# Kernel optimization log

Hardware: AMD Instinct MI355X
Metric: run time of the kernel (lower is better)

The kernel has to match this reference:

```python
import jax, jax.numpy as jnp
import numpy as np

B, N, D = 4096, 64, 12
SS = 5            # self_state_dim
I = D - SS        # lstm input dim = 7
H = 256           # hn_state_dim
M1, M2 = 512, 512 # mlp_dims
A = 81            # n_actions


def setup_inputs() -> dict:
    key = jax.random.key(0)
    ks = jax.random.split(key, 12)
    w = lambda k, shape: (jax.random.normal(k, shape, jnp.float32) * 0.05)
    return {
        "state": jax.random.normal(ks[0], (B, N, D), jnp.float32),
        "W_ih": w(ks[1], (4 * H, I)),
        "W_hh": w(ks[2], (4 * H, H)),
        "b_ih": w(ks[3], (4 * H,)),
        "b_hh": w(ks[4], (4 * H,)),
        "W1": w(ks[5], (SS + H, M1)),
        "b1": w(ks[6], (M1,)),
        "W2": w(ks[7], (M1, M2)),
        "b2": w(ks[8], (M2,)),
        "Wv": w(ks[9], (M2, A)),
        "bv": w(ks[10], (A,)),
    }


def reference(state, W_ih, W_hh, b_ih, b_hh, W1, b1, W2, b2, Wv, bv):
    self_state = state[:, 0, :SS]                      # [B, SS]
    # dist: inf when either of coords 5,6 is zero (faithful to np.all(..)==0 quirk)
    s5, s6 = state[..., 5], state[..., 6]
    d = jnp.where((s5 != 0) & (s6 != 0),
                  jnp.sqrt(s5 * s5 + s6 * s6), jnp.inf)  # [B, N]
    order = jnp.argsort(-d, axis=1)                    # stable desc sort by dist
    sorted_state = jnp.take_along_axis(state, order[..., None], axis=1)
    x = sorted_state[:, :, SS:]                        # [B, N, I]

    def step(carry, xt):
        h, c = carry
        g = xt @ W_ih.T + b_ih + h @ W_hh.T + b_hh     # [B, 4H]
        i, f, gg, o = jnp.split(g, 4, axis=-1)
        c = jax.nn.sigmoid(f) * c + jax.nn.sigmoid(i) * jnp.tanh(gg)
        h = jax.nn.sigmoid(o) * jnp.tanh(c)
        return (h, c), None

    h0 = jnp.zeros((state.shape[0], H), state.dtype)
    (hn, _), _ = jax.lax.scan(step, (h0, h0), jnp.swapaxes(x, 0, 1))

    joint = jnp.concatenate([self_state, hn], axis=1)  # [B, SS+H]
    out = jax.nn.relu(joint @ W1 + b1)
    out = jax.nn.relu(out @ W2 + b2)                   # last_relu=True
    values = out @ Wv + bv                             # [B, A]
    return values
```

## Files before the change

kernel.cpp:

```cpp
#include <hip/hip_runtime.h>
#include <math.h>

#define B_   4096
#define N_   64
#define SS_  5
#define I_   7
#define H_   256
#define M1_  512
#define M2_  512
#define A_   81

typedef _Float16 f16;
typedef f16   f16x8 __attribute__((ext_vector_type(8)));
typedef float f32x4 __attribute__((ext_vector_type(4)));
typedef int   i32x4 __attribute__((ext_vector_type(4)));

__device__ __forceinline__ float sigm_(float x) {
  return __builtin_amdgcn_rcpf(1.f + __expf(-x));
}
__device__ __forceinline__ float tanh_(float x) {
  return 1.f - 2.f * __builtin_amdgcn_rcpf(__expf(2.f * x) + 1.f);
}

__global__ __launch_bounds__(1024) void pack_weights(
    const float* __restrict__ W_ih,
    const float* __restrict__ W_hh,
    const float* __restrict__ b_ih,
    const float* __restrict__ b_hh,
    const float* __restrict__ W1,
    const float* __restrict__ W2,
    const float* __restrict__ Wv,
    signed char* __restrict__ Wq2,
    signed char* __restrict__ Wql2,
    f16* __restrict__ Wxk,
    float* __restrict__ scd,
    f16* __restrict__ Wp1,
    f16* __restrict__ Wp2,
    f16* __restrict__ Wpv) {
  const int gtid = blockIdx.x * 1024 + threadIdx.x;

  if (gtid < 65536) {
    const int p    = gtid >> 6;
    const int lane = gtid & 63;
    const int w16 = p >> 6, r = p & 63, g = r >> 4, uu = r & 15;
    const int row = g * H_ + w16 * 16 + uu;

    const float4 v4 = *(const float4*)(W_hh + row * H_ + lane * 4);
    float mx = fmaxf(fmaxf(fabsf(v4.x), fabsf(v4.y)),
                     fmaxf(fabsf(v4.z), fabsf(v4.w)));
    #pragma unroll
    for (int off = 32; off; off >>= 1)
      mx = fmaxf(mx, __shfl_xor(mx, off));
    mx = fmaxf(mx, 1e-12f);
    const float is = 127.f / mx;

    int b0i = (int)rintf(v4.x * is), b1i = (int)rintf(v4.y * is);
    int b2i = (int)rintf(v4.z * is), b3i = (int)rintf(v4.w * is);
    b0i = max(-127, min(127, b0i)); b1i = max(-127, min(127, b1i));
    b2i = max(-127, min(127, b2i)); b3i = max(-127, min(127, b3i));
    const unsigned int packed = (b0i & 0xff) | ((b1i & 0xff) << 8) |
                                ((b2i & 0xff) << 16) | ((b3i & 0xff) << 24);
    const int k    = lane * 4;
    const int kt2  = k >> 6;
    const int kk   = k & 63;
    *(unsigned int*)(Wq2 + kt2 * 65536 + p * 64 + kk) = packed;

    if (kt2 < 2) {
      const int lgk = kk >> 4;
      const int jq  = kk & 15;
      *(unsigned int*)(Wql2 + ((kt2 * 16 + w16) * 4 + g) * 1024 +
                       lgk * 256 + uu * 16 + jq) = packed;
    }

    if (lane < 8) {
      f16 v;
      if (lane < I_)      v = (f16)W_ih[row * I_ + lane];
      else                v = (f16)(b_ih[row] + b_hh[row]);
      Wxk[p * 8 + lane] = v;
    }
    if (lane == 9)  scd[p] = mx * (1.f / 16129.f);
  }

  if (gtid < 288 * 512) {
    const int k = gtid >> 9, n = gtid & 511;
    const int kt = k >> 5, lg = (k >> 3) & 3, j = k & 7;
    const int nt = n >> 4, l15 = n & 15;
    const float v = (k < 261) ? W1[k * 512 + n] : 0.f;
    Wp1[(((kt * 32 + nt) * 16 + l15) * 4 + lg) * 8 + j] = (f16)v;
  }
  if (gtid < 512 * 512) {
    const int k = gtid >> 9, n = gtid & 511;
    const int kt = k >> 5, lg = (k >> 3) & 3, j = k & 7;
    const int nt = n >> 4, l15 = n & 15;
    Wp2[(((kt * 32 + nt) * 16 + l15) * 4 + lg) * 8 + j] = (f16)W2[k * 512 + n];
  }
  if (gtid < 512 * 96) {
    const int k = gtid / 96, n = gtid - k * 96;
    const int kt = k >> 5, lg = (k >> 3) & 3, j = k & 7;
    const int nt = n >> 4, l15 = n & 15;
    const float v = (n < A_) ? Wv[k * A_ + n] : 0.f;
    Wpv[(((kt * 6 + nt) * 16 + l15) * 4 + lg) * 8 + j] = (f16)v;
  }
}

__global__ void sort_gather(const float* __restrict__ state,
                            f16* __restrict__ xbuf,
                            float* __restrict__ selfbuf) {
  const int b = blockIdx.x;
  const int e = threadIdx.x;
  const float* row = state + ((size_t)b * N_ + e) * 12;
  const float4* r4 = (const float4*)row;
  const float4 v0 = r4[0], v1 = r4[1], v2 = r4[2];
  float s[12];
  s[0]=v0.x; s[1]=v0.y; s[2]=v0.z;  s[3]=v0.w;
  s[4]=v1.x; s[5]=v1.y; s[6]=v1.z;  s[7]=v1.w;
  s[8]=v2.x; s[9]=v2.y; s[10]=v2.z; s[11]=v2.w;

  const float s5 = s[5], s6 = s[6];
  const float d = (s5 != 0.f && s6 != 0.f) ? sqrtf(s5 * s5 + s6 * s6) : INFINITY;

  __shared__ float dd[64];
  dd[e] = d;
  __syncthreads();

  int rank = 0;
  #pragma unroll
  for (int j = 0; j < 64; ++j) {
    const float dj = dd[j];
    rank += (dj > d || (dj == d && j < e)) ? 1 : 0;
  }

  f16* xo = xbuf + (((size_t)(b >> 4) * 64 + rank) * 16 + (b & 15)) * 8;
  #pragma unroll
  for (int f = 0; f < I_; ++f) xo[f] = (f16)s[SS_ + f];
  xo[7] = (f16)1.f;

  if (e == 0) {
    #pragma unroll
    for (int i = 0; i < SS_; ++i) selfbuf[b * SS_ + i] = s[i];
  }
}

__global__ __attribute__((amdgpu_flat_work_group_size(1024, 1024)))
void lstm_kernel(
    const f16* __restrict__ xbuf,
    const signed char* __restrict__ Wq2,
    const signed char* __restrict__ Wql2,
    const f16* __restrict__ Wxk,
    const float* __restrict__ scd,
    float* __restrict__ hnbuf) {
  const int tid = threadIdx.x;
  const int l   = tid & 63;
  const int w   = tid >> 6;
  const int l15 = l & 15;
  const int lg  = l >> 4;
  const int b0  = blockIdx.x << 4;

  extern __shared__ char smem[];
  signed char* Wl_s = (signed char*)smem;
  f16*   Bx_s  = (f16*)(smem + 131072);
  signed char* hq_s = (signed char*)(smem + 147456);
  f16*   x_s   = (f16*)(smem + 155648);

  {
    const f16x8* sw = (const f16x8*)Wql2;
    f16x8* dw = (f16x8*)Wl_s;
    for (int i = tid; i < 8192; i += 1024) dw[i] = sw[i];
    const f16x8* sx = (const f16x8*)Wxk;
    f16x8* dx = (f16x8*)Bx_s;
    for (int i = tid; i < 1024; i += 1024) dx[i] = sx[i];
    for (int i = tid; i < 2048; i += 1024) ((int*)hq_s)[i] = 0;
    if (tid < 128) x_s[tid] = xbuf[(size_t)blockIdx.x * 8192 + tid];
  }

  float scv[4][4];
  #pragma unroll
  for (int g = 0; g < 4; ++g)
    #pragma unroll
    for (int e = 0; e < 4; ++e)
      scv[g][e] = scd[w * 64 + g * 16 + lg * 4 + e];

  const int WLB = w * 4096 + l * 16;
  const int SB  = w * 4096 + l15 * 64 + lg * 16;
  const int BXB = w * 1024 + l15 * 16;
  const int u0  = w * 16 + lg * 4;
  const int HW  = w * 256 + l15 * 16 + lg * 4;
  const int HR  = l * 16;

  i32x4 Bs[2][4];
  #pragma unroll
  for (int m = 0; m < 2; ++m)
    #pragma unroll
    for (int g = 0; g < 4; ++g)
      Bs[m][g] = *(const i32x4*)(Wq2 + (2 + m) * 65536 + g * 1024 + SB);

  float c_[4] = {0.f, 0.f, 0.f, 0.f};

  __syncthreads();

  #pragma unroll 1
  for (int t = 0; t < 64; ++t) {
    int z = 0;
    asm volatile("" : "+v"(z));
    const int wlb = WLB + z;
    const int hrb = HR + ((t & 1) * 4096) + z;
    const int bxb = BXB + z;

    f16 xn = (f16)0.f;
    if (tid < 128) {
      const int tn = (t < 63) ? t + 1 : 63;
      xn = xbuf[(size_t)blockIdx.x * 8192 + tn * 128 + tid];
    }

    f16x8 bx = {(f16)0.f,(f16)0.f,(f16)0.f,(f16)0.f,
                (f16)0.f,(f16)0.f,(f16)0.f,(f16)0.f};
    if (lg == 0) bx = *(const f16x8*)&x_s[(t & 1) * 128 + l15 * 8];

    i32x4 acc[4];
    #pragma unroll
    for (int g = 0; g < 4; ++g) acc[g] = (i32x4){0, 0, 0, 0};

    #pragma unroll
    for (int kt2 = 0; kt2 < 2; ++kt2) {
      const i32x4 Hf = *(const i32x4*)&hq_s[hrb + kt2 * 1024];
      #pragma unroll
      for (int g = 0; g < 4; ++g) {
        const i32x4 Wv = *(const i32x4*)(Wl_s + kt2 * 65536 + g * 1024 + wlb);
        acc[g] = __builtin_amdgcn_mfma_i32_16x16x64_i8(Wv, Hf, acc[g], 0, 0, 0);
      }
    }
    #pragma unroll
    for (int m = 0; m < 2; ++m) {
      const i32x4 Hf = *(const i32x4*)&hq_s[hrb + (2 + m) * 1024];
      #pragma unroll
      for (int g = 0; g < 4; ++g)
        acc[g] = __builtin_amdgcn_mfma_i32_16x16x64_i8(Bs[m][g], Hf, acc[g], 0, 0, 0);
    }

    f32x4 facc[4];
    #pragma unroll
    for (int g = 0; g < 4; ++g) {
      f32x4 accF = (f32x4){0.f, 0.f, 0.f, 0.f};
      const f16x8 Wxv = *(const f16x8*)((const char*)Bx_s + bxb + g * 256);
      accF = __builtin_amdgcn_mfma_f32_16x16x32_f16(Wxv, bx, accF, 0, 0, 0);
      #pragma unroll
      for (int e = 0; e < 4; ++e)
        facc[g][e] = (float)acc[g][e] * scv[g][e] + accF[e];
    }

    float hv[4];
    #pragma unroll
    for (int e = 0; e < 4; ++e) {
      const float gi = facc[0][e];
      const float gf = facc[1][e];
      const float gg = facc[2][e];
      const float go = facc[3][e];
      const float cn = sigm_(gf) * c_[e] + sigm_(gi) * tanh_(gg);
      c_[e] = cn;
      hv[e] = sigm_(go) * tanh_(cn);
    }
    const int q0 = (int)rintf(hv[0] * 127.f) & 255;
    const int q1 = (int)rintf(hv[1] * 127.f) & 255;
    const int q2 = (int)rintf(hv[2] * 127.f) & 255;
    const int q3 = (int)rintf(hv[3] * 127.f) & 255;
    *(unsigned int*)(hq_s + ((t + 1) & 1) * 4096 + HW) =
        (unsigned int)(q0 | (q1 << 8) | (q2 << 16) | (q3 << 24));
    if (t == 63) {
      float4 hx = {hv[0], hv[1], hv[2], hv[3]};
      *(float4*)&hnbuf[(size_t)(b0 + l15) * H_ + u0] = hx;
    }
    if (tid < 128) x_s[((t + 1) & 1) * 128 + tid] = xn;
    __syncthreads();
  }
}

__global__ __launch_bounds__(512) void mlp_kernel(
    const float* __restrict__ selfb, const float* __restrict__ hnbuf,
    const f16* __restrict__ Wp1, const float* __restrict__ b1,
    const f16* __restrict__ Wp2, const float* __restrict__ b2,
    const f16* __restrict__ Wpv, const float* __restrict__ bv,
    float* __restrict__ out) {
  const int tid = threadIdx.x;
  const int l   = tid & 63;
  const int w   = tid >> 6;
  const int l15 = l & 15;
  const int lg  = l >> 4;
  const int b0  = blockIdx.x << 5;

  extern __shared__ char smem[];
  f16* aA = (f16*)smem;
  f16* aB = (f16*)(smem + 18944);
  f16* aC = (f16*)(smem + 18944 + 33280);

  for (int i = tid; i < 32 * 296; i += 512) {
    const int r = i / 296, cc = i - r * 296;
    float v = 0.f;
    if (cc < SS_)        v = selfb[(b0 + r) * SS_ + cc];
    else if (cc < 261)   v = hnbuf[((size_t)(b0 + r)) * H_ + cc - SS_];
    aA[i] = (f16)v;
  }
  __syncthreads();

  f32x4 acc[2][4];

  {
    #pragma unroll
    for (int mt = 0; mt < 2; ++mt)
      #pragma unroll
      for (int nt4 = 0; nt4 < 4; ++nt4) acc[mt][nt4] = (f32x4){0.f,0.f,0.f,0.f};
    for (int kt = 0; kt < 9; ++kt) {
      const f16x8 A0 = *(const f16x8*)&aA[(l15) * 296 + kt * 32 + lg * 8];
      const f16x8 A1 = *(const f16x8*)&aA[(16 + l15) * 296 + kt * 32 + lg * 8];
      #pragma unroll
      for (int nt4 = 0; nt4 < 4; ++nt4) {
        const int nt = w * 4 + nt4;
        const f16x8 Bv = *(const f16x8*)(Wp1 + (((kt * 32 + nt) * 16 + l15) * 4 + lg) * 8);
        acc[0][nt4] = __builtin_amdgcn_mfma_f32_16x16x32_f16(A0, Bv, acc[0][nt4], 0, 0, 0);
        acc[1][nt4] = __builtin_amdgcn_mfma_f32_16x16x32_f16(A1, Bv, acc[1][nt4], 0, 0, 0);
      }
    }
    #pragma unroll
    for (int nt4 = 0; nt4 < 4; ++nt4) {
      const int n = (w * 4 + nt4) * 16 + l15;
      const float bb = b1[n];
      #pragma unroll
      for (int mt = 0; mt < 2; ++mt)
        #pragma unroll
        for (int e = 0; e < 4; ++e) {
          const float v = fmaxf(acc[mt][nt4][e] + bb, 0.f);
          aB[(mt * 16 + lg * 4 + e) * 520 + n] = (f16)v;
        }
    }
  }
  __syncthreads();

  {
    #pragma unroll
    for (int mt = 0; mt < 2; ++mt)
      #pragma unroll
      for (int nt4 = 0; nt4 < 4; ++nt4) acc[mt][nt4] = (f32x4){0.f,0.f,0.f,0.f};
    for (int kt = 0; kt < 16; ++kt) {
      const f16x8 A0 = *(const f16x8*)&aB[(l15) * 520 + kt * 32 + lg * 8];
      const f16x8 A1 = *(const f16x8*)&aB[(16 + l15) * 520 + kt * 32 + lg * 8];
      #pragma unroll
      for (int nt4 = 0; nt4 < 4; ++nt4) {
        const int nt = w * 4 + nt4;
        const f16x8 Bv = *(const f16x8*)(Wp2 + (((kt * 32 + nt) * 16 + l15) * 4 + lg) * 8);
        acc[0][nt4] = __builtin_amdgcn_mfma_f32_16x16x32_f16(A0, Bv, acc[0][nt4], 0, 0, 0);
        acc[1][nt4] = __builtin_amdgcn_mfma_f32_16x16x32_f16(A1, Bv, acc[1][nt4], 0, 0, 0);
      }
    }
    #pragma unroll
    for (int nt4 = 0; nt4 < 4; ++nt4) {
      const int n = (w * 4 + nt4) * 16 + l15;
      const float bb = b2[n];
      #pragma unroll
      for (int mt = 0; mt < 2; ++mt)
        #pragma unroll
        for (int e = 0; e < 4; ++e) {
          const float v = fmaxf(acc[mt][nt4][e] + bb, 0.f);
          aC[(mt * 16 + lg * 4 + e) * 520 + n] = (f16)v;
        }
    }
  }
  __syncthreads();

  if (w < 6) {
    const int n = w * 16 + l15;
    f32x4 acc3[2];
    acc3[0] = (f32x4){0.f,0.f,0.f,0.f};
    acc3[1] = (f32x4){0.f,0.f,0.f,0.f};
    for (int kt = 0; kt < 16; ++kt) {
      const f16x8 A0 = *(const f16x8*)&aC[(l15) * 520 + kt * 32 + lg * 8];
      const f16x8 A1 = *(const f16x8*)&aC[(16 + l15) * 520 + kt * 32 + lg * 8];
      const f16x8 Bv = *(const f16x8*)(Wpv + (((kt * 6 + w) * 16 + l15) * 4 + lg) * 8);
      acc3[0] = __builtin_amdgcn_mfma_f32_16x16x32_f16(A0, Bv, acc3[0], 0, 0, 0);
      acc3[1] = __builtin_amdgcn_mfma_f32_16x16x32_f16(A1, Bv, acc3[1], 0, 0, 0);
    }
    if (n < A_) {
      const float bb = bv[n];
      #pragma unroll
      for (int mt = 0; mt < 2; ++mt)
        #pragma unroll
        for (int e = 0; e < 4; ++e)
          out[(size_t)(b0 + mt * 16 + lg * 4 + e) * A_ + n] = acc3[mt][e] + bb;
    }
  }
}

extern "C" void kernel_launch(void* const* d_in, const int* in_sizes, int n_in,
                              void* d_out, int out_size, void* d_ws, size_t ws_size,
                              hipStream_t stream) {
  const float* state = (const float*)d_in[0];
  const float* W_ih  = (const float*)d_in[1];
  const float* W_hh  = (const float*)d_in[2];
  const float* b_ih  = (const float*)d_in[3];
  const float* b_hh  = (const float*)d_in[4];
  const float* W1    = (const float*)d_in[5];
  const float* b1    = (const float*)d_in[6];
  const float* W2    = (const float*)d_in[7];
  const float* b2    = (const float*)d_in[8];
  const float* Wv    = (const float*)d_in[9];
  const float* bv    = (const float*)d_in[10];
  float* out = (float*)d_out;

  char* ws = (char*)d_ws;
  signed char* Wq2  = (signed char*)(ws);
  signed char* Wql2 = (signed char*)(ws + 262144);
  f16*   Wxk     = (f16*)(ws + 393216);
  float* scd     = (float*)(ws + 413696);
  f16*   xbuf    = (f16*)(ws + 417792);
  float* selfb   = (float*)(ws + 4612096);
  float* hnbuf   = (float*)(ws + 4694016);
  f16*   Wp1     = (f16*)(ws + 8888320);
  f16*   Wp2     = (f16*)(ws + 9183232);
  f16*   Wpv     = (f16*)(ws + 9707520);

  pack_weights<<<dim3(256), dim3(1024), 0, stream>>>(
      W_ih, W_hh, b_ih, b_hh, W1, W2, Wv,
      Wq2, Wql2, Wxk, scd, Wp1, Wp2, Wpv);
  sort_gather<<<dim3(B_), dim3(64), 0, stream>>>(state, xbuf, selfb);
  lstm_kernel<<<dim3(B_ / 16), dim3(1024), 156160, stream>>>(xbuf, Wq2, Wql2,
                                                             Wxk, scd, hnbuf);
  mlp_kernel<<<dim3(B_ / 32), dim3(512), 85504, stream>>>(selfb, hnbuf,
                                                          Wp1, b1, Wp2, b2,
                                                          Wpv, bv, out);
}
```

Before: 172.4 us.

## Keep all int8 recurrent weights in registers instead of shared memory

The LSTM kernel now loads all four K-slices of the int8 W_hh fragments into registers (64 VGPRs' worth of i32x4) and drops the 128KB shared-memory weight copy and its repacking in pack_weights. This removes per-step LDS weight reads and shrinks shared memory from about 156KB to 25KB, which could allow more blocks per CU. It also replaces the rintf-based quantisation of h with a magic-number fmaf rounding trick. The cost is higher register pressure with 1024-thread blocks, which risks spills.

```diff
diff --git a/kernel.cpp b/kernel.cpp
--- a/kernel.cpp
+++ b/kernel.cpp
@@ -31,7 +31,6 @@
     const float* __restrict__ W2,
     const float* __restrict__ Wv,
     signed char* __restrict__ Wq2,
-    signed char* __restrict__ Wql2,
     f16* __restrict__ Wxk,
     float* __restrict__ scd,
     f16* __restrict__ Wp1,
@@ -64,13 +63,6 @@
     const int kt2  = k >> 6;
     const int kk   = k & 63;
     *(unsigned int*)(Wq2 + kt2 * 65536 + p * 64 + kk) = packed;
-
-    if (kt2 < 2) {
-      const int lgk = kk >> 4;
-      const int jq  = kk & 15;
-      *(unsigned int*)(Wql2 + ((kt2 * 16 + w16) * 4 + g) * 1024 +
-                       lgk * 256 + uu * 16 + jq) = packed;
-    }
 
     if (lane < 8) {
       f16 v;
@@ -145,7 +137,6 @@
 void lstm_kernel(
     const f16* __restrict__ xbuf,
     const signed char* __restrict__ Wq2,
-    const signed char* __restrict__ Wql2,
     const f16* __restrict__ Wxk,
     const float* __restrict__ scd,
     float* __restrict__ hnbuf) {
@@ -157,15 +148,11 @@
   const int b0  = blockIdx.x << 4;
 
   extern __shared__ char smem[];
-  signed char* Wl_s = (signed char*)smem;
-  f16*   Bx_s  = (f16*)(smem + 131072);
-  signed char* hq_s = (signed char*)(smem + 147456);
-  f16*   x_s   = (f16*)(smem + 155648);
+  f16*   Bx_s  = (f16*)smem;
+  signed char* hq_s = (signed char*)(smem + 16384);
+  f16*   x_s   = (f16*)(smem + 24576);
 
   {
-    const f16x8* sw = (const f16x8*)Wql2;
-    f16x8* dw = (f16x8*)Wl_s;
-    for (int i = tid; i < 8192; i += 1024) dw[i] = sw[i];
     const f16x8* sx = (const f16x8*)Wxk;
     f16x8* dx = (f16x8*)Bx_s;
     for (int i = tid; i < 1024; i += 1024) dx[i] = sx[i];
@@ -180,19 +167,18 @@
     for (int e = 0; e < 4; ++e)
       scv[g][e] = scd[w * 64 + g * 16 + lg * 4 + e];
 
-  const int WLB = w * 4096 + l * 16;
   const int SB  = w * 4096 + l15 * 64 + lg * 16;
   const int BXB = w * 1024 + l15 * 16;
   const int u0  = w * 16 + lg * 4;
   const int HW  = w * 256 + l15 * 16 + lg * 4;
   const int HR  = l * 16;
 
-  i32x4 Bs[2][4];
+  i32x4 Bq[4][4];
   #pragma unroll
-  for (int m = 0; m < 2; ++m)
+  for (int kt2 = 0; kt2 < 4; ++kt2)
     #pragma unroll
     for (int g = 0; g < 4; ++g)
-      Bs[m][g] = *(const i32x4*)(Wq2 + (2 + m) * 65536 + g * 1024 + SB);
+      Bq[kt2][g] = *(const i32x4*)(Wq2 + kt2 * 65536 + g * 1024 + SB);
 
   float c_[4] = {0.f, 0.f, 0.f, 0.f};
 
@@ -202,8 +188,7 @@
   for (int t = 0; t < 64; ++t) {
     int z = 0;
     asm volatile("" : "+v"(z));
-    const int wlb = WLB + z;
-    const int hrb = HR + ((t & 1) * 4096) + z;
+    const int hrb = HR + ((t & 1) * 4096);
     const int bxb = BXB + z;
 
     f16 xn = (f16)0.f;
@@ -221,20 +206,11 @@
     for (int g = 0; g < 4; ++g) acc[g] = (i32x4){0, 0, 0, 0};
 
     #pragma unroll
-    for (int kt2 = 0; kt2 < 2; ++kt2) {
+    for (int kt2 = 0; kt2 < 4; ++kt2) {
       const i32x4 Hf = *(const i32x4*)&hq_s[hrb + kt2 * 1024];
       #pragma unroll
-      for (int g = 0; g < 4; ++g) {
-        const i32x4 Wv = *(const i32x4*)(Wl_s + kt2 * 65536 + g * 1024 + wlb);
-        acc[g] = __builtin_amdgcn_mfma_i32_16x16x64_i8(Wv, Hf, acc[g], 0, 0, 0);
-      }
-    }
-    #pragma unroll
-    for (int m = 0; m < 2; ++m) {
-      const i32x4 Hf = *(const i32x4*)&hq_s[hrb + (2 + m) * 1024];
-      #pragma unroll
       for (int g = 0; g < 4; ++g)
-        acc[g] = __builtin_amdgcn_mfma_i32_16x16x64_i8(Bs[m][g], Hf, acc[g], 0, 0, 0);
+        acc[g] = __builtin_amdgcn_mfma_i32_16x16x64_i8(Bq[kt2][g], Hf, acc[g], 0, 0, 0);
     }
 
     f32x4 facc[4];
@@ -259,12 +235,12 @@
       c_[e] = cn;
       hv[e] = sigm_(go) * tanh_(cn);
     }
-    const int q0 = (int)rintf(hv[0] * 127.f) & 255;
-    const int q1 = (int)rintf(hv[1] * 127.f) & 255;
-    const int q2 = (int)rintf(hv[2] * 127.f) & 255;
-    const int q3 = (int)rintf(hv[3] * 127.f) & 255;
+    const unsigned mg0 = __float_as_uint(fmaf(hv[0], 127.f, 12582912.f));
+    const unsigned mg1 = __float_as_uint(fmaf(hv[1], 127.f, 12582912.f));
+    const unsigned mg2 = __float_as_uint(fmaf(hv[2], 127.f, 12582912.f));
+    const unsigned mg3 = __float_as_uint(fmaf(hv[3], 127.f, 12582912.f));
     *(unsigned int*)(hq_s + ((t + 1) & 1) * 4096 + HW) =
-        (unsigned int)(q0 | (q1 << 8) | (q2 << 16) | (q3 << 24));
+        (mg0 & 255u) | ((mg1 & 255u) << 8) | ((mg2 & 255u) << 16) | (mg3 << 24);
     if (t == 63) {
       float4 hx = {hv[0], hv[1], hv[2], hv[3]};
       *(float4*)&hnbuf[(size_t)(b0 + l15) * H_ + u0] = hx;
@@ -406,22 +382,21 @@
 
   char* ws = (char*)d_ws;
   signed char* Wq2  = (signed char*)(ws);
-  signed char* Wql2 = (signed char*)(ws + 262144);
-  f16*   Wxk     = (f16*)(ws + 393216);
-  float* scd     = (float*)(ws + 413696);
-  f16*   xbuf    = (f16*)(ws + 417792);
-  float* selfb   = (float*)(ws + 4612096);
-  float* hnbuf   = (float*)(ws + 4694016);
-  f16*   Wp1     = (f16*)(ws + 8888320);
-  f16*   Wp2     = (f16*)(ws + 9183232);
-  f16*   Wpv     = (f16*)(ws + 9707520);
+  f16*   Wxk     = (f16*)(ws + 262144);
+  float* scd     = (float*)(ws + 278528);
+  f16*   xbuf    = (f16*)(ws + 282624);
+  float* selfb   = (float*)(ws + 4476928);
+  float* hnbuf   = (float*)(ws + 4558848);
+  f16*   Wp1     = (f16*)(ws + 8753152);
+  f16*   Wp2     = (f16*)(ws + 9048064);
+  f16*   Wpv     = (f16*)(ws + 9572352);
 
   pack_weights<<<dim3(256), dim3(1024), 0, stream>>>(
       W_ih, W_hh, b_ih, b_hh, W1, W2, Wv,
-      Wq2, Wql2, Wxk, scd, Wp1, Wp2, Wpv);
+      Wq2, Wxk, scd, Wp1, Wp2, Wpv);
   sort_gather<<<dim3(B_), dim3(64), 0, stream>>>(state, xbuf, selfb);
-  lstm_kernel<<<dim3(B_ / 16), dim3(1024), 156160, stream>>>(xbuf, Wq2, Wql2,
-                                                             Wxk, scd, hnbuf);
+  lstm_kernel<<<dim3(B_ / 16), dim3(1024), 25088, stream>>>(xbuf, Wq2, Wxk,
+                                                            scd, hnbuf);
   mlp_kernel<<<dim3(B_ / 32), dim3(512), 85504, stream>>>(selfb, hnbuf,
                                                           Wp1, b1, Wp2, b2,
                                                           Wpv, bv, out);
```

Result: no change. 172.8 us (+0.3%).
